# Kernel tuning notes

Measured on AMD Instinct MI355X. Metric: run time of the kernel, lower is better.

The kernel has to match this reference:

```python
import jax, jax.numpy as jnp
import numpy as np

DEPTH = 2
D_MODEL = 768
D_STATE = 64
EXPAND = 2
D_CONV = 4
D_INNER = EXPAND * D_MODEL          # 1536
DT_RANK = (D_MODEL + 15) // 16      # 48
BATCH, SEQ = 4, 2048


def setup_inputs() -> dict:
    key = jax.random.key(0)
    ks = jax.random.split(key, 8)
    s = 0.02  # small init scale for stability
    return {
        "x": jax.random.normal(ks[0], (BATCH, SEQ, D_MODEL), jnp.float32),
        # per-layer params stacked along leading DEPTH axis
        "in_proj_w": jax.random.normal(ks[1], (DEPTH, 2 * D_INNER, D_MODEL), jnp.float32) * s,
        "conv_w": jax.random.normal(ks[2], (DEPTH, D_INNER, D_CONV), jnp.float32) * s,
        "conv_b": jnp.zeros((DEPTH, D_INNER), jnp.float32),
        "x_proj_w": jax.random.normal(ks[3], (DEPTH, DT_RANK + 2 * D_STATE, D_INNER), jnp.float32) * s,
        "dt_proj_w": jax.random.normal(ks[4], (DEPTH, D_INNER, DT_RANK), jnp.float32) * s,
        "dt_proj_b": jax.random.normal(ks[5], (DEPTH, D_INNER), jnp.float32) * s,
        # S4D-real init: A = -[1..N] per channel -> A_log = log(arange)
        "A_log": jnp.tile(jnp.log(jnp.arange(1, D_STATE + 1, dtype=jnp.float32))[None, None, :],
                          (DEPTH, D_INNER, 1)),
        "D_skip": jnp.ones((DEPTH, D_INNER), jnp.float32),
        "out_proj_w": jax.random.normal(ks[6], (DEPTH, D_MODEL, D_INNER), jnp.float32) * s,
    }


def _causal_conv1d(x, w, b):
    # depthwise causal conv: x [B,L,d], w [d,K], b [d]
    L = x.shape[1]
    xp = jnp.pad(x, ((0, 0), (D_CONV - 1, 0), (0, 0)))
    y = b
    for k in range(D_CONV):
        y = y + xp[:, k:k + L, :] * w[:, k]
    return y


def _selective_scan(u, dt, A, Bm, Cm):
    # u, dt: [B,L,d]; A: [d,N]; Bm, Cm: [B,L,N]
    def step(h, inp):
        dt_t, B_t, C_t, u_t = inp  # [B,d],[B,N],[B,N],[B,d]
        dA = jnp.exp(dt_t[..., None] * A)                         # [B,d,N]
        h = dA * h + dt_t[..., None] * B_t[:, None, :] * u_t[..., None]
        y_t = jnp.einsum('bdn,bn->bd', h, C_t)
        return h, y_t

    h0 = jnp.zeros((u.shape[0], u.shape[2], A.shape[1]), u.dtype)
    xs = (jnp.swapaxes(dt, 0, 1), jnp.swapaxes(Bm, 0, 1),
          jnp.swapaxes(Cm, 0, 1), jnp.swapaxes(u, 0, 1))
    _, ys = jax.lax.scan(step, h0, xs)  # ys [L,B,d]
    return jnp.swapaxes(ys, 0, 1)


def _mamba_layer(x, Wi, cw, cb, Wx, Wdt, bdt, A_log, Dp, Wo):
    xz = x @ Wi.T                                  # [B,L,2*d_inner]
    xpart, z = jnp.split(xz, 2, axis=-1)
    xpart = jax.nn.silu(_causal_conv1d(xpart, cw, cb))
    xdbl = xpart @ Wx.T                            # [B,L,dt_rank+2N]
    dt_in, Bm, Cm = jnp.split(xdbl, [DT_RANK, DT_RANK + D_STATE], axis=-1)
    dt = jax.nn.softplus(dt_in @ Wdt.T + bdt)      # [B,L,d_inner]
    A = -jnp.exp(A_log)                            # [d_inner, N]
    y = _selective_scan(xpart, dt, A, Bm, Cm) + Dp * xpart
    y = y * jax.nn.silu(z)
    return y @ Wo.T                                # [B,L,d_model]


def reference(x, in_proj_w, conv_w, conv_b, x_proj_w, dt_proj_w, dt_proj_b,
              A_log, D_skip, out_proj_w):
    for i in range(DEPTH):
        x = _mamba_layer(x, in_proj_w[i], conv_w[i], conv_b[i], x_proj_w[i],
                         dt_proj_w[i], dt_proj_b[i], A_log[i], D_skip[i],
                         out_proj_w[i])
    return x
```

## Files before the change

### kernel.cpp

```cpp
#include <hip/hip_runtime.h>
#include <hip/hip_bf16.h>
#include <math.h>

#define DEPTH   2
#define DM      768
#define DS      64
#define DC      4
#define DI      1536
#define DTR     48
#define BATCH   4
#define SEQ     2048
#define MROWS   (BATCH*SEQ)
#define XDC     (DTR + 2*DS)
#define NC      8
#define TCH     (SEQ/NC)
#define LOG2E   1.44269504088896f

typedef __attribute__((ext_vector_type(8))) short bf16x8;
typedef __attribute__((ext_vector_type(4))) float f32x4;
typedef __attribute__((ext_vector_type(2))) float f32x2;
typedef __attribute__((ext_vector_type(2))) unsigned int uint2v;
typedef unsigned short ushort_t;
#define GAS __attribute__((address_space(1)))
#define LAS __attribute__((address_space(3)))

__device__ __forceinline__ float silu_fast(float x) {
    return x / (1.f + __expf(-x));
}
__device__ __forceinline__ float softplus_acc(float x) {
    return x > 20.f ? x : log1pf(expf(x));
}

__device__ __forceinline__ ushort_t bf16_hi(float f) {
    unsigned u = __float_as_uint(f);
    unsigned hr = u + 0x7FFF + ((u >> 16) & 1);
    return (ushort_t)(hr >> 16);
}

__device__ __forceinline__ f32x2 merge_x32_2(f32x2 a, f32x2 b) {
#if __has_builtin(__builtin_amdgcn_permlane32_swap)
    const uint2v rx = __builtin_amdgcn_permlane32_swap(
        __float_as_uint(a.x), __float_as_uint(b.x), false, false);
    const uint2v ry = __builtin_amdgcn_permlane32_swap(
        __float_as_uint(a.y), __float_as_uint(b.y), false, false);
    const f32x2 s0 = {__uint_as_float(rx[0]), __uint_as_float(ry[0])};
    const f32x2 s1 = {__uint_as_float(rx[1]), __uint_as_float(ry[1])};
    return s0 + s1;
#else
    const f32x2 sa = {a.x + __shfl_xor(a.x, 32, 64), a.y + __shfl_xor(a.y, 32, 64)};
    const f32x2 sb = {b.x + __shfl_xor(b.x, 32, 64), b.y + __shfl_xor(b.y, 32, 64)};
    return (threadIdx.x & 32) ? sb : sa;
#endif
}

__device__ __forceinline__ f32x2 merge_x16_2(f32x2 a, f32x2 b) {
#if __has_builtin(__builtin_amdgcn_permlane16_swap)
    const uint2v rx = __builtin_amdgcn_permlane16_swap(
        __float_as_uint(a.x), __float_as_uint(b.x), false, false);
    const uint2v ry = __builtin_amdgcn_permlane16_swap(
        __float_as_uint(a.y), __float_as_uint(b.y), false, false);
    const f32x2 s0 = {__uint_as_float(rx[0]), __uint_as_float(ry[0])};
    const f32x2 s1 = {__uint_as_float(rx[1]), __uint_as_float(ry[1])};
    return s0 + s1;
#else
    const f32x2 sa = {a.x + __shfl_xor(a.x, 16, 64), a.y + __shfl_xor(a.y, 16, 64)};
    const f32x2 sb = {b.x + __shfl_xor(b.x, 16, 64), b.y + __shfl_xor(b.y, 16, 64)};
    return (threadIdx.x & 16) ? sb : sa;
#endif
}

template <int CTRL>
__device__ __forceinline__ f32x2 dpp_add2(f32x2 x) {
    const int tx = __builtin_amdgcn_update_dpp(
        0, __float_as_int(x.x), CTRL, 0xF, 0xF, true);
    const int ty = __builtin_amdgcn_update_dpp(
        0, __float_as_int(x.y), CTRL, 0xF, 0xF, true);
    const f32x2 t = {__int_as_float(tx), __int_as_float(ty)};
    return x + t;
}
__device__ __forceinline__ f32x2 rowsum16_2(f32x2 x) {
    x = dpp_add2<0x128>(x);
    x = dpp_add2<0x124>(x);
    x = dpp_add2<0x122>(x);
    x = dpp_add2<0x121>(x);
    return x;
}

__global__ __launch_bounds__(256) void quant_bf16(
    const float* __restrict__ in, ushort_t* __restrict__ hi)
{
    const size_t i = ((size_t)blockIdx.x * 256 + threadIdx.x) * 4;
    const float4 v = *(const float4*)(in + i);
    ushort4 h;
    h.x = bf16_hi(v.x); h.y = bf16_hi(v.y);
    h.z = bf16_hi(v.z); h.w = bf16_hi(v.w);
    *(ushort4*)(hi + i) = h;
}

__global__ __launch_bounds__(256, 2) void gemm_mfma(
    const ushort_t* __restrict__ A, const ushort_t* __restrict__ W,
    float* __restrict__ C, int N, int K, int ldA, int ldW,
    ushort_t* __restrict__ Chi, float4* __restrict__ bc4out, int mode)
{
    __shared__ ushort_t lds[2][128 * 32];
    const int tid  = threadIdx.x;
    const int wave = tid >> 6, lane = tid & 63;

    int bx = blockIdx.x, by = blockIdx.y;
    {
        const int X   = gridDim.x;
        const int fid = by * X + bx;
        const int xcd = fid & 7;
        const int j   = fid >> 3;
        const int jX  = j / X;
        by = xcd * (gridDim.y >> 3) + jX;
        bx = j - jX * X;
    }
    const int bm0 = by * 128, bn0 = bx * 128;
    const int wm = (wave >> 1) * 64, wn = (wave & 1) * 64;

    const int srow = lane >> 2;
    const int skq  = (lane & 3) * 8;

    f32x4 acc[4][4];
#pragma unroll
    for (int i = 0; i < 4; i++)
#pragma unroll
        for (int j = 0; j < 4; j++) acc[i][j] = (f32x4){0.f, 0.f, 0.f, 0.f};

    const int lm  = lane & 15;
    const int kg8 = (lane >> 4) * 8;

    for (int k0 = 0; k0 < K; k0 += 32) {
#pragma unroll
        for (int j = 0; j < 4; j++) {
            const int ldid = wave * 4 + j;
            const int buf  = ldid >> 3;
            const int slot = ldid & 7;
            const ushort_t* gsrc = buf ? W : A;
            const int ldg = buf ? ldW : ldA;
            const int rb  = buf ? bn0 : bm0;
            const ushort_t* ga = gsrc + (size_t)(rb + slot * 16 + srow) * ldg + k0 + skq;
            __builtin_amdgcn_global_load_lds(
                (const GAS unsigned*)ga, (LAS unsigned*)&lds[buf][slot * 512], 16, 0, 0);
        }
        __syncthreads();

        bf16x8 ah[4], bh[4];
#pragma unroll
        for (int i = 0; i < 4; i++) {
            const int ar = (wm + i * 16 + lm) * 32 + kg8;
            ah[i] = *(const bf16x8*)&lds[0][ar];
            const int br = (wn + i * 16 + lm) * 32 + kg8;
            bh[i] = *(const bf16x8*)&lds[1][br];
        }
#pragma unroll
        for (int mi = 0; mi < 4; mi++)
#pragma unroll
            for (int ni = 0; ni < 4; ni++)
                acc[mi][ni] = __builtin_amdgcn_mfma_f32_16x16x32_bf16(
                    ah[mi], bh[ni], acc[mi][ni], 0, 0, 0);
        __syncthreads();
    }

#pragma unroll
    for (int mi = 0; mi < 4; mi++)
#pragma unroll
        for (int ni = 0; ni < 4; ni++) {
            const int rowb = bm0 + wm + mi * 16 + (lane >> 4) * 4;
            const int colg = bn0 + wn + ni * 16 + lm;
            if (mode == 1) {
#pragma unroll
                for (int r = 0; r < 4; r++)
                    Chi[(size_t)(rowb + r) * N + colg] = bf16_hi(acc[mi][ni][r]);
            } else if (mode == 2) {
                if (colg >= DTR && colg < DTR + 2 * DS) {
                    const f32x4 a = acc[mi][ni];
                    bc4out[(size_t)(rowb >> 2) * 128 + (colg - DTR)] =
                        make_float4(a[0], a[1], a[2], a[3]);
                } else if (colg < DTR) {
#pragma unroll
                    for (int r = 0; r < 4; r++)
                        C[(size_t)(rowb + r) * N + colg] = acc[mi][ni][r];
                }
            } else {
#pragma unroll
                for (int r = 0; r < 4; r++)
                    if (colg < N)
                        C[(size_t)(rowb + r) * N + colg] = acc[mi][ni][r];
            }
        }
}

__global__ __launch_bounds__(256, 2) void gemm_dt_T(
    const float* __restrict__ Wdt, const float* __restrict__ xdbl,
    const float* __restrict__ bias, float* __restrict__ dtT)
{
    __shared__ float As[8][132];
    __shared__ float Bs[8][132];
    const int tid = threadIdx.x;
    const int bd0 = blockIdx.y * 128;
    const int bt0 = blockIdx.x * 128;
    const int b   = blockIdx.z;
    const int tx = tid & 15;
    const int ty = tid >> 4;
    const int lrow = tid >> 1;
    const int lk4  = (tid & 1) * 4;

    float acc[8][8];
#pragma unroll
    for (int i = 0; i < 8; i++)
#pragma unroll
        for (int j = 0; j < 8; j++) acc[i][j] = 0.f;

    for (int k0 = 0; k0 < DTR; k0 += 8) {
        const float4 av = *(const float4*)(Wdt + (size_t)(bd0 + lrow) * DTR + k0 + lk4);
        const float4 wv = *(const float4*)(xdbl + ((size_t)b * SEQ + bt0 + lrow) * XDC + k0 + lk4);
        __syncthreads();
        As[lk4 + 0][lrow] = av.x; As[lk4 + 1][lrow] = av.y;
        As[lk4 + 2][lrow] = av.z; As[lk4 + 3][lrow] = av.w;
        Bs[lk4 + 0][lrow] = wv.x; Bs[lk4 + 1][lrow] = wv.y;
        Bs[lk4 + 2][lrow] = wv.z; Bs[lk4 + 3][lrow] = wv.w;
        __syncthreads();
#pragma unroll
        for (int kk = 0; kk < 8; kk++) {
            const float4 a0 = *(const float4*)&As[kk][ty * 8];
            const float4 a1 = *(const float4*)&As[kk][ty * 8 + 4];
            const float4 b0 = *(const float4*)&Bs[kk][tx * 8];
            const float4 b1 = *(const float4*)&Bs[kk][tx * 8 + 4];
            const float ar[8] = {a0.x, a0.y, a0.z, a0.w, a1.x, a1.y, a1.z, a1.w};
            const float br[8] = {b0.x, b0.y, b0.z, b0.w, b1.x, b1.y, b1.z, b1.w};
#pragma unroll
            for (int i = 0; i < 8; i++)
#pragma unroll
                for (int j = 0; j < 8; j++)
                    acc[i][j] = fmaf(ar[i], br[j], acc[i][j]);
        }
    }

#pragma unroll
    for (int i = 0; i < 8; i++) {
        const int d = bd0 + ty * 8 + i;
        const float bb = bias[d];
#pragma unroll
        for (int j4 = 0; j4 < 8; j4 += 4) {
            float4 v = make_float4(acc[i][j4], acc[i][j4 + 1], acc[i][j4 + 2], acc[i][j4 + 3]);
            v.x = softplus_acc(v.x + bb);
            v.y = softplus_acc(v.y + bb);
            v.z = softplus_acc(v.z + bb);
            v.w = softplus_acc(v.w + bb);
            *(float4*)(dtT + ((size_t)b * DI + d) * SEQ + bt0 + tx * 8 + j4) = v;
        }
    }
}

__global__ __launch_bounds__(256) void conv_silu_T2(
    const float* __restrict__ xz, const float* __restrict__ cw,
    const float* __restrict__ cb, float* __restrict__ uT,
    ushort_t* __restrict__ uh)
{
    __shared__ float tin[67][65];
    __shared__ float ttr[64][65];
    const int tid = threadIdx.x;
    const int d0 = blockIdx.x * 64, t0 = blockIdx.y * 64, b = blockIdx.z;
    const int cl = tid & 63, q = tid >> 6;

    for (int r = q; r < 67; r += 4) {
        const int t = t0 - 3 + r;
        float v = 0.f;
        if (t >= 0) v = xz[((size_t)b * SEQ + t) * (2 * DI) + d0 + cl];
        tin[r][cl] = v;
    }
    __syncthreads();

    const float4 w = ((const float4*)cw)[d0 + cl];
    const float bb = cb[d0 + cl];
#pragma unroll
    for (int i = 0; i < 16; i++) {
        const int t = q * 16 + i;
        float a = bb;
        a = fmaf(tin[t + 0][cl], w.x, a);
        a = fmaf(tin[t + 1][cl], w.y, a);
        a = fmaf(tin[t + 2][cl], w.z, a);
        a = fmaf(tin[t + 3][cl], w.w, a);
        a = silu_fast(a);
        ttr[cl][t] = a;
        const size_t row = (size_t)b * SEQ + t0 + t;
        uh[row * DI + d0 + cl] = bf16_hi(a);
    }
    __syncthreads();
#pragma unroll
    for (int i = 0; i < 16; i++) {
        const int d = q * 16 + i;
        uT[((size_t)b * DI + d0 + d) * SEQ + t0 + cl] = ttr[d][cl];
    }
}


__global__ __launch_bounds__(256, 2) void scan_tail(
    const float* __restrict__ dtT, const float* __restrict__ uT,
    const float4* __restrict__ bc4, const float* __restrict__ A_log,
    float* __restrict__ hend)
{
    const int wid  = __builtin_amdgcn_readfirstlane(
                        (int)((blockIdx.x * 256 + threadIdx.x) >> 6));
    const int lane = threadIdx.x & 63;
    const int c  = wid & (NC - 1);
    const int bd = wid >> 3;
    const int b  = bd / DI;
    const int d  = bd - b * DI;

    const float An = -expf(A_log[d * DS + lane]) * LOG2E;
    const float* dtp = dtT + (size_t)bd * SEQ + c * TCH;
    const float* up  = uT  + (size_t)bd * SEQ + c * TCH;
    const float4* Bp = bc4 + ((size_t)b * (SEQ / 4) + c * (TCH / 4)) * 128 + lane;

    float h = 0.f, r = 0.f;
    for (int tb = TCH - 16; tb >= 0; tb -= 16) {
        float4 dt4[4], u4[4], B4[4];
#pragma unroll
        for (int g = 0; g < 4; g++) {
            dt4[g] = *(const float4*)(dtp + tb + 4 * g);
            u4[g]  = *(const float4*)(up  + tb + 4 * g);
            B4[g]  = Bp[(size_t)(tb / 4 + g) * 128];
        }
#pragma unroll
        for (int g = 3; g >= 0; g--) {
            h = fmaf(__builtin_amdgcn_exp2f(An * r), (dt4[g].w * u4[g].w) * B4[g].w, h); r += dt4[g].w;
            h = fmaf(__builtin_amdgcn_exp2f(An * r), (dt4[g].z * u4[g].z) * B4[g].z, h); r += dt4[g].z;
            h = fmaf(__builtin_amdgcn_exp2f(An * r), (dt4[g].y * u4[g].y) * B4[g].y, h); r += dt4[g].y;
            h = fmaf(__builtin_amdgcn_exp2f(An * r), (dt4[g].x * u4[g].x) * B4[g].x, h); r += dt4[g].x;
        }
        if (__all(An * r < -30.f)) break;
    }
    hend[(size_t)wid * DS + lane] = h;
}

__global__ __launch_bounds__(256) void scan_phase2(
    const float* __restrict__ dtT, const float* __restrict__ A_log,
    const float* __restrict__ hend, float* __restrict__ h0out)
{
    const int bd   = (blockIdx.x * 256 + threadIdx.x) >> 6;
    const int lane = threadIdx.x & 63;
    const int d    = bd % DI;

    const float* dtp = dtT + (size_t)bd * SEQ + lane * 32;
    float s = 0.f;
#pragma unroll
    for (int g = 0; g < 8; g++) {
        const float4 v = *(const float4*)(dtp + 4 * g);
        s += (v.x + v.y) + (v.z + v.w);
    }
    s += __shfl_xor(s, 1, 64);
    s += __shfl_xor(s, 2, 64);
    s += __shfl_xor(s, 4, 64);

    const float An = -expf(A_log[d * DS + lane]) * LOG2E;
    float h = 0.f;
#pragma unroll
    for (int c = 0; c < NC; c++) {
        const float sdt = __shfl(s, 8 * c, 64);
        const size_t off = ((size_t)bd * NC + c) * DS + lane;
        h0out[off] = h;
        h = fmaf(__builtin_amdgcn_exp2f(An * sdt), h, hend[off]);
    }
}


#define LOAD6(D0, D1, U0, U1, BB_, CC_, TB)                            \
    _Pragma("unroll")                                                  \
    for (int g = 0; g < 4; g++) {                                      \
        D0[g]  = *(const float4*)(dtp0 + (TB) + 4 * g);                \
        D1[g]  = *(const float4*)(dtp1 + (TB) + 4 * g);                \
        U0[g]  = *(const float4*)(up0 + (TB) + 4 * g);                 \
        U1[g]  = *(const float4*)(up1 + (TB) + 4 * g);                 \
        BB_[g] = Bp[(size_t)((TB) / 4 + g) * 128];                     \
        CC_[g] = Cp[(size_t)((TB) / 4 + g) * 128];                     \
    }

#define P3_STEP(E, G, D0, D1, U0, U1, BB_, CC_, LF)                    \
    {                                                                  \
        const f32x2 dte = {D0[G].E, D1[G].E};                          \
        const f32x2 ue  = {U0[G].E, U1[G].E};                          \
        f32x2 w2 = dte * An2;                                          \
        const f32x2 ee = {__builtin_amdgcn_exp2f(w2.x),                \
                          __builtin_amdgcn_exp2f(w2.y)};               \
        const f32x2 p2 = (dte * ue) * BB_[G].E;                        \
        h2 = ee * h2 + p2;                                             \
        LF = h2 * CC_[G].E;                                            \
    }

#define P3_BLOCK(D0, D1, U0, U1, BB_, CC_, TBASE)                      \
    {                                                                  \
        f32x2 m[8];                                                    \
        _Pragma("unroll")                                              \
        for (int g = 0; g < 4; g++) {                                  \
            f32x2 lf0, lf1, lf2, lf3;                                  \
            P3_STEP(x, g, D0, D1, U0, U1, BB_, CC_, lf0)               \
            P3_STEP(y, g, D0, D1, U0, U1, BB_, CC_, lf1)               \
            P3_STEP(z, g, D0, D1, U0, U1, BB_, CC_, lf2)               \
            P3_STEP(w, g, D0, D1, U0, U1, BB_, CC_, lf3)               \
            m[2 * g]     = merge_x32_2(lf0, lf1);                      \
            m[2 * g + 1] = merge_x32_2(lf2, lf3);                      \
        }                                                              \
        const f32x2 q0 = rowsum16_2(merge_x16_2(m[0], m[1]));          \
        const f32x2 q1 = rowsum16_2(merge_x16_2(m[2], m[3]));          \
        const f32x2 q2 = rowsum16_2(merge_x16_2(m[4], m[5]));          \
        const f32x2 q3 = rowsum16_2(merge_x16_2(m[6], m[7]));          \
        const f32x2 v = (lane & 2) ? ((lane & 1) ? q3 : q2)            \
                                   : ((lane & 1) ? q1 : q0);           \
        if ((lane & 15) < 4) {                                         \
            sp0[(TBASE) + wtt] = v.x;                                  \
            sp1[(TBASE) + wtt] = v.y;                                  \
        }                                                              \
    }

__global__ __launch_bounds__(256, 2) void scan_phase3(
    const float* __restrict__ dtT, const float* __restrict__ uT,
    const float4* __restrict__ bc4, const float* __restrict__ A_log,
    const float* __restrict__ hin, float* __restrict__ sX)
{
    const int tid  = threadIdx.x;
    const int wid  = __builtin_amdgcn_readfirstlane(
                        (int)((blockIdx.x * 256 + tid) >> 6));
    const int lane = tid & 63;
    const int c   = wid & (NC - 1);
    const int bdq = wid >> 3;
    const int bd0 = bdq * 2;
    const int b   = bd0 / DI;
    const int d0  = bd0 - b * DI;

    const f32x2 An2 = {-expf(A_log[(size_t)d0 * DS + lane]) * LOG2E,
                       -expf(A_log[(size_t)(d0 + 1) * DS + lane]) * LOG2E};

    const float* dtp0 = dtT + (size_t)bd0 * SEQ + c * TCH;
    const float* dtp1 = dtp0 + SEQ;
    const float* up0  = uT  + (size_t)bd0 * SEQ + c * TCH;
    const float* up1  = up0 + SEQ;
    const float4* Bp = bc4 + ((size_t)b * (SEQ / 4) + c * (TCH / 4)) * 128 + lane;
    const float4* Cp = Bp + 64;

    const size_t L0 = (size_t)bd0 * SEQ + c * TCH;
    const size_t L1 = L0 + SEQ;
    float* sp0 = sX + (L0 / 1536) * 3072 + (L0 % 1536);
    float* sp1 = sX + (L1 / 1536) * 3072 + (L1 % 1536);

    const int wr  = lane >> 4;
    const int wtt = 4 * (lane & 3) + (((wr & 1) << 1) | (wr >> 1));

    f32x2 h2 = {hin[((size_t)bd0 * NC + c) * DS + lane],
                hin[((size_t)(bd0 + 1) * NC + c) * DS + lane]};

    float4 dA0[4], dA1[4], uA0[4], uA1[4], BA4[4], CA4[4];
    float4 dB0[4], dB1[4], uB0[4], uB1[4], BB4[4], CB4[4];
    LOAD6(dA0, dA1, uA0, uA1, BA4, CA4, 0);

    for (int tb = 0; tb < TCH; tb += 32) {
        LOAD6(dB0, dB1, uB0, uB1, BB4, CB4, tb + 16);
        P3_BLOCK(dA0, dA1, uA0, uA1, BA4, CA4, tb);
        LOAD6(dA0, dA1, uA0, uA1, BA4, CA4, tb + 32);
        P3_BLOCK(dB0, dB1, uB0, uB1, BB4, CB4, tb + 16);
    }
}

__global__ __launch_bounds__(256) void gate_split_T(
    const float* __restrict__ xz, const float* __restrict__ uT,
    const float* __restrict__ Dskip, ushort_t* __restrict__ yh)
{
    __shared__ float zt[64][65];
    __shared__ float yt[64][65];
    const int tid = threadIdx.x;
    const int d0 = blockIdx.x * 64, t0 = blockIdx.y * 64, b = blockIdx.z;
    const int cl = tid & 63, q = tid >> 6;
#pragma unroll
    for (int i = 0; i < 16; i++) {
        const int r = q * 16 + i;
        zt[r][cl] = xz[((size_t)b * SEQ + t0 + r) * (2 * DI) + DI + d0 + cl];
    }
    __syncthreads();
#pragma unroll
    for (int i = 0; i < 16; i++) {
        const int dd = q * 16 + i;
        const size_t Lrow = ((size_t)b * DI + d0 + dd) * SEQ + t0;
        const float s = xz[(Lrow / 1536) * 3072 + (Lrow % 1536) + cl];
        const float u = uT[Lrow + cl];
        const float Dd = Dskip[d0 + dd];
        yt[dd][cl] = (s + Dd * u) * silu_fast(zt[cl][dd]);
    }
    __syncthreads();
#pragma unroll
    for (int i = 0; i < 16; i++) {
        const int t = q * 16 + i;
        const size_t row = (size_t)b * SEQ + t0 + t;
        yh[row * DI + d0 + cl] = bf16_hi(yt[cl][t]);
    }
}

extern "C" void kernel_launch(void* const* d_in, const int* in_sizes, int n_in,
                              void* d_out, int out_size, void* d_ws, size_t ws_size,
                              hipStream_t stream) {
    (void)in_sizes; (void)n_in; (void)out_size; (void)ws_size;
    const float* x    = (const float*)d_in[0];
    const float* Wi   = (const float*)d_in[1];
    const float* cw   = (const float*)d_in[2];
    const float* cb   = (const float*)d_in[3];
    const float* Wx   = (const float*)d_in[4];
    const float* Wdt  = (const float*)d_in[5];
    const float* bdt  = (const float*)d_in[6];
    const float* Alog = (const float*)d_in[7];
    const float* Dsk  = (const float*)d_in[8];
    const float* Wo   = (const float*)d_in[9];
    float* out = (float*)d_out;

    float* xz    = (float*)d_ws;
    float* uT    = xz    + (size_t)MROWS * (2 * DI);
    float* dtT   = uT    + (size_t)MROWS * DI;
    float* xdbl  = dtT   + (size_t)MROWS * DI;
    float* bcT   = xdbl  + (size_t)MROWS * XDC;
    float* xnext = bcT   + (size_t)BATCH * 128 * SEQ;
    float* hend  = xnext;
    float* h0buf = xnext + (size_t)BATCH * DI * NC * DS;

    ushort_t* sh  = (ushort_t*)uT;
    ushort_t* wih = (ushort_t*)(dtT + (size_t)MROWS * DM);
    ushort_t* uh  = (ushort_t*)dtT;
    ushort_t* wxh = (ushort_t*)xnext;
    ushort_t* woh = (ushort_t*)xdbl;
    ushort_t* yh  = (ushort_t*)xnext;

    for (int i = 0; i < DEPTH; i++) {
        const float* Wi_l   = Wi   + (size_t)i * 2 * DI * DM;
        const float* cw_l   = cw   + (size_t)i * DI * DC;
        const float* cb_l   = cb   + (size_t)i * DI;
        const float* Wx_l   = Wx   + (size_t)i * XDC * DI;
        const float* Wdt_l  = Wdt  + (size_t)i * DI * DTR;
        const float* bdt_l  = bdt  + (size_t)i * DI;
        const float* Alog_l = Alog + (size_t)i * DI * DS;
        const float* Dsk_l  = Dsk  + (size_t)i * DI;
        const float* Wo_l   = Wo   + (size_t)i * DM * DI;

        if (i == 0)
            quant_bf16<<<(size_t)MROWS * DM / 1024, 256, 0, stream>>>(x, sh);
        quant_bf16<<<(size_t)2 * DI * DM / 1024, 256, 0, stream>>>(Wi_l, wih);
        gemm_mfma<<<dim3(2 * DI / 128, MROWS / 128), 256, 0, stream>>>(
            sh, wih, xz, 2 * DI, DM, DM, DM, nullptr, nullptr, 0);
        conv_silu_T2<<<dim3(DI / 64, SEQ / 64, BATCH), 256, 0, stream>>>(
            xz, cw_l, cb_l, uT, uh);
        quant_bf16<<<(size_t)XDC * DI / 1024, 256, 0, stream>>>(Wx_l, wxh);
        gemm_mfma<<<dim3((XDC + 127) / 128, MROWS / 128), 256, 0, stream>>>(
            uh, wxh, xdbl, XDC, DI, DI, DI, nullptr, (float4*)bcT, 2);
        gemm_dt_T<<<dim3(SEQ / 128, DI / 128, BATCH), 256, 0, stream>>>(
            Wdt_l, xdbl, bdt_l, dtT);
        scan_tail<<<(BATCH * DI * NC) / 4, 256, 0, stream>>>(
            dtT, uT, (const float4*)bcT, Alog_l, hend);
        scan_phase2<<<(BATCH * DI) / 4, 256, 0, stream>>>(
            dtT, Alog_l, hend, h0buf);
        scan_phase3<<<(BATCH * DI * NC) / 8, 256, 0, stream>>>(
            dtT, uT, (const float4*)bcT, Alog_l, h0buf, xz);
        gate_split_T<<<dim3(DI / 64, SEQ / 64, BATCH), 256, 0, stream>>>(
            xz, uT, Dsk_l, yh);
        quant_bf16<<<(size_t)DM * DI / 1024, 256, 0, stream>>>(Wo_l, woh);
        if (i == DEPTH - 1)
            gemm_mfma<<<dim3(DM / 128, MROWS / 128), 256, 0, stream>>>(
                yh, woh, out, DM, DI, DI, DI, nullptr, nullptr, 0);
        else
            gemm_mfma<<<dim3(DM / 128, MROWS / 128), 256, 0, stream>>>(
                yh, woh, xz , DM, DI, DI, DI, sh, nullptr, 1);
    }
}
```

Baseline: 1.115 ms.

## Store in_proj output as bf16 and process two channels per wave in scan_tail

The in_proj GEMM now writes its xz output directly as bf16 through the existing bf16-output mode. The conv and gate kernels read that bf16 buffer, and the scan output moves to a separate contiguous fp32 buffer. This halves xz write and read traffic and simplifies scan-output indexing. scan_tail now handles two d channels per wavefront with paired f32x2 math and launches half as many blocks, reusing B loads and raising ILP. The trade-off is added bf16 rounding on the x and z activations before the conv and gating.

Measured after the change: 1.241 ms. 1.11x slower.

```diff
diff --git a/kernel.cpp b/kernel.cpp
--- a/kernel.cpp
+++ b/kernel.cpp
@@ -35,6 +35,9 @@
     unsigned u = __float_as_uint(f);
     unsigned hr = u + 0x7FFF + ((u >> 16) & 1);
     return (ushort_t)(hr >> 16);
+}
+__device__ __forceinline__ float bf16_f32(ushort_t u) {
+    return __uint_as_float((unsigned)u << 16);
 }
 
 __device__ __forceinline__ f32x2 merge_x32_2(f32x2 a, f32x2 b) {
@@ -255,7 +258,7 @@
 }
 
 __global__ __launch_bounds__(256) void conv_silu_T2(
-    const float* __restrict__ xz, const float* __restrict__ cw,
+    const ushort_t* __restrict__ xzh, const float* __restrict__ cw,
     const float* __restrict__ cb, float* __restrict__ uT,
     ushort_t* __restrict__ uh)
 {
@@ -268,7 +271,7 @@
     for (int r = q; r < 67; r += 4) {
         const int t = t0 - 3 + r;
         float v = 0.f;
-        if (t >= 0) v = xz[((size_t)b * SEQ + t) * (2 * DI) + d0 + cl];
+        if (t >= 0) v = bf16_f32(xzh[((size_t)b * SEQ + t) * (2 * DI) + d0 + cl]);
         tin[r][cl] = v;
     }
     __syncthreads();
@@ -297,6 +300,17 @@
 }
 
 
+#define TAIL_STEP(E, G)                                                \
+    {                                                                  \
+        const f32x2 dte = {dt0[G].E, dt1[G].E};                        \
+        const f32x2 ue  = {u0v[G].E, u1v[G].E};                        \
+        const f32x2 w2  = An2 * r2;                                    \
+        const f32x2 ee  = {__builtin_amdgcn_exp2f(w2.x),               \
+                           __builtin_amdgcn_exp2f(w2.y)};              \
+        h2 = h2 + ee * ((dte * ue) * B4[G].E);                         \
+        r2 = r2 + dte;                                                 \
+    }
+
 __global__ __launch_bounds__(256, 2) void scan_tail(
     const float* __restrict__ dtT, const float* __restrict__ uT,
     const float4* __restrict__ bc4, const float* __restrict__ A_log,
@@ -305,35 +319,42 @@
     const int wid  = __builtin_amdgcn_readfirstlane(
                         (int)((blockIdx.x * 256 + threadIdx.x) >> 6));
     const int lane = threadIdx.x & 63;
-    const int c  = wid & (NC - 1);
-    const int bd = wid >> 3;
-    const int b  = bd / DI;
-    const int d  = bd - b * DI;
-
-    const float An = -expf(A_log[d * DS + lane]) * LOG2E;
-    const float* dtp = dtT + (size_t)bd * SEQ + c * TCH;
-    const float* up  = uT  + (size_t)bd * SEQ + c * TCH;
+    const int c   = wid & (NC - 1);
+    const int bdq = wid >> 3;
+    const int bd0 = bdq * 2;
+    const int b   = bd0 / DI;
+    const int d0  = bd0 - b * DI;
+
+    const f32x2 An2 = {-expf(A_log[(size_t)d0 * DS + lane]) * LOG2E,
+                       -expf(A_log[(size_t)(d0 + 1) * DS + lane]) * LOG2E};
+    const float* dtp0 = dtT + (size_t)bd0 * SEQ + c * TCH;
+    const float* dtp1 = dtp0 + SEQ;
+    const float* up0  = uT  + (size_t)bd0 * SEQ + c * TCH;
+    const float* up1  = up0 + SEQ;
     const float4* Bp = bc4 + ((size_t)b * (SEQ / 4) + c * (TCH / 4)) * 128 + lane;
 
-    float h = 0.f, r = 0.f;
+    f32x2 h2 = {0.f, 0.f}, r2 = {0.f, 0.f};
     for (int tb = TCH - 16; tb >= 0; tb -= 16) {
-        float4 dt4[4], u4[4], B4[4];
+        float4 dt0[4], dt1[4], u0v[4], u1v[4], B4[4];
 #pragma unroll
         for (int g = 0; g < 4; g++) {
-            dt4[g] = *(const float4*)(dtp + tb + 4 * g);
-            u4[g]  = *(const float4*)(up  + tb + 4 * g);
+            dt0[g] = *(const float4*)(dtp0 + tb + 4 * g);
+            dt1[g] = *(const float4*)(dtp1 + tb + 4 * g);
+            u0v[g] = *(const float4*)(up0 + tb + 4 * g);
+            u1v[g] = *(const float4*)(up1 + tb + 4 * g);
             B4[g]  = Bp[(size_t)(tb / 4 + g) * 128];
         }
 #pragma unroll
         for (int g = 3; g >= 0; g--) {
-            h = fmaf(__builtin_amdgcn_exp2f(An * r), (dt4[g].w * u4[g].w) * B4[g].w, h); r += dt4[g].w;
-            h = fmaf(__builtin_amdgcn_exp2f(An * r), (dt4[g].z * u4[g].z) * B4[g].z, h); r += dt4[g].z;
-            h = fmaf(__builtin_amdgcn_exp2f(An * r), (dt4[g].y * u4[g].y) * B4[g].y, h); r += dt4[g].y;
-            h = fmaf(__builtin_amdgcn_exp2f(An * r), (dt4[g].x * u4[g].x) * B4[g].x, h); r += dt4[g].x;
-        }
-        if (__all(An * r < -30.f)) break;
-    }
-    hend[(size_t)wid * DS + lane] = h;
+            TAIL_STEP(w, g)
+            TAIL_STEP(z, g)
+            TAIL_STEP(y, g)
+            TAIL_STEP(x, g)
+        }
+        if (__all((An2.x * r2.x < -30.f) && (An2.y * r2.y < -30.f))) break;
+    }
+    hend[((size_t)bd0 * NC + c) * DS + lane]       = h2.x;
+    hend[((size_t)(bd0 + 1) * NC + c) * DS + lane] = h2.y;
 }
 
 __global__ __launch_bounds__(256) void scan_phase2(
@@ -440,10 +461,8 @@
     const float4* Bp = bc4 + ((size_t)b * (SEQ / 4) + c * (TCH / 4)) * 128 + lane;
     const float4* Cp = Bp + 64;
 
-    const size_t L0 = (size_t)bd0 * SEQ + c * TCH;
-    const size_t L1 = L0 + SEQ;
-    float* sp0 = sX + (L0 / 1536) * 3072 + (L0 % 1536);
-    float* sp1 = sX + (L1 / 1536) * 3072 + (L1 % 1536);
+    float* sp0 = sX + (size_t)bd0 * SEQ + c * TCH;
+    float* sp1 = sp0 + SEQ;
 
     const int wr  = lane >> 4;
     const int wtt = 4 * (lane & 3) + (((wr & 1) << 1) | (wr >> 1));
@@ -464,8 +483,9 @@
 }
 
 __global__ __launch_bounds__(256) void gate_split_T(
-    const float* __restrict__ xz, const float* __restrict__ uT,
-    const float* __restrict__ Dskip, ushort_t* __restrict__ yh)
+    const ushort_t* __restrict__ xzh, const float* __restrict__ sbuf,
+    const float* __restrict__ uT, const float* __restrict__ Dskip,
+    ushort_t* __restrict__ yh)
 {
     __shared__ float zt[64][65];
     __shared__ float yt[64][65];
@@ -475,14 +495,14 @@
 #pragma unroll
     for (int i = 0; i < 16; i++) {
         const int r = q * 16 + i;
-        zt[r][cl] = xz[((size_t)b * SEQ + t0 + r) * (2 * DI) + DI + d0 + cl];
+        zt[r][cl] = bf16_f32(xzh[((size_t)b * SEQ + t0 + r) * (2 * DI) + DI + d0 + cl]);
     }
     __syncthreads();
 #pragma unroll
     for (int i = 0; i < 16; i++) {
         const int dd = q * 16 + i;
         const size_t Lrow = ((size_t)b * DI + d0 + dd) * SEQ + t0;
-        const float s = xz[(Lrow / 1536) * 3072 + (Lrow % 1536) + cl];
+        const float s = sbuf[Lrow + cl];
         const float u = uT[Lrow + cl];
         const float Dd = Dskip[d0 + dd];
         yt[dd][cl] = (s + Dd * u) * silu_fast(zt[cl][dd]);
@@ -512,8 +532,9 @@
     const float* Wo   = (const float*)d_in[9];
     float* out = (float*)d_out;
 
-    float* xz    = (float*)d_ws;
-    float* uT    = xz    + (size_t)MROWS * (2 * DI);
+    ushort_t* xzh = (ushort_t*)d_ws;
+    float* sbuf  = (float*)d_ws + (size_t)MROWS * 1536;
+    float* uT    = (float*)d_ws + (size_t)MROWS * 3072;
     float* dtT   = uT    + (size_t)MROWS * DI;
     float* xdbl  = dtT   + (size_t)MROWS * DI;
     float* bcT   = xdbl  + (size_t)MROWS * XDC;
@@ -543,28 +564,28 @@
             quant_bf16<<<(size_t)MROWS * DM / 1024, 256, 0, stream>>>(x, sh);
         quant_bf16<<<(size_t)2 * DI * DM / 1024, 256, 0, stream>>>(Wi_l, wih);
         gemm_mfma<<<dim3(2 * DI / 128, MROWS / 128), 256, 0, stream>>>(
-            sh, wih, xz, 2 * DI, DM, DM, DM, nullptr, nullptr, 0);
+            sh, wih, nullptr, 2 * DI, DM, DM, DM, xzh, nullptr, 1);
         conv_silu_T2<<<dim3(DI / 64, SEQ / 64, BATCH), 256, 0, stream>>>(
-            xz, cw_l, cb_l, uT, uh);
+            xzh, cw_l, cb_l, uT, uh);
         quant_bf16<<<(size_t)XDC * DI / 1024, 256, 0, stream>>>(Wx_l, wxh);
         gemm_mfma<<<dim3((XDC + 127) / 128, MROWS / 128), 256, 0, stream>>>(
             uh, wxh, xdbl, XDC, DI, DI, DI, nullptr, (float4*)bcT, 2);
         gemm_dt_T<<<dim3(SEQ / 128, DI / 128, BATCH), 256, 0, stream>>>(
             Wdt_l, xdbl, bdt_l, dtT);
-        scan_tail<<<(BATCH * DI * NC) / 4, 256, 0, stream>>>(
+        scan_tail<<<(BATCH * DI * NC) / 8, 256, 0, stream>>>(
             dtT, uT, (const float4*)bcT, Alog_l, hend);
         scan_phase2<<<(BATCH * DI) / 4, 256, 0, stream>>>(
             dtT, Alog_l, hend, h0buf);
         scan_phase3<<<(BATCH * DI * NC) / 8, 256, 0, stream>>>(
-            dtT, uT, (const float4*)bcT, Alog_l, h0buf, xz);
+            dtT, uT, (const float4*)bcT, Alog_l, h0buf, sbuf);
         gate_split_T<<<dim3(DI / 64, SEQ / 64, BATCH), 256, 0, stream>>>(
-            xz, uT, Dsk_l, yh);
+            xzh, sbuf, uT, Dsk_l, yh);
         quant_bf16<<<(size_t)DM * DI / 1024, 256, 0, stream>>>(Wo_l, woh);
         if (i == DEPTH - 1)
             gemm_mfma<<<dim3(DM / 128, MROWS / 128), 256, 0, stream>>>(
                 yh, woh, out, DM, DI, DI, DI, nullptr, nullptr, 0);
         else
             gemm_mfma<<<dim3(DM / 128, MROWS / 128), 256, 0, stream>>>(
-                yh, woh, xz , DM, DI, DI, DI, sh, nullptr, 1);
-    }
-}
+                yh, woh, nullptr, DM, DI, DI, DI, sh, nullptr, 1);
+    }
+}
```
